# Optimization experiments

Hardware: AMD Instinct MI355X
Metric: run time of the kernel (lower is better)

Reference implementation:

```python
import jax, jax.numpy as jnp
import numpy as np

NG, NC, FG, FC, D = 8192, 4096, 512, 256, 64
ALPHA = 0.2          # leaky_relu negative slope
NEG = -9.0e15        # mask fill value from the torch code


def _leaky(x):
    return jnp.where(x >= 0, x, ALPHA * x)


def _relation(h_src, h_dst, a, adj):
    # additive GAT score: e[i,j] = leaky(h_src[i]@a[:D] + h_dst[j]@a[D:])
    s1 = h_src @ a[:D]            # [Ns]
    s2 = h_dst @ a[D:]            # [Nd]
    e = _leaky(s1[:, None] + s2[None, :])          # [Ns, Nd]
    att = jax.nn.softmax(jnp.where(adj > 0, e, NEG), axis=1)
    return att @ h_dst            # [Ns, D]


def setup_inputs() -> dict:
    key = jax.random.key(0)
    ks = jax.random.split(key, 14)
    sc = 0.05
    return {
        "gene_x": jax.random.normal(ks[0], (NG, FG), jnp.float32),
        "cell_x": jax.random.normal(ks[1], (NC, FC), jnp.float32),
        "W_g": jax.random.normal(ks[2], (FG, D), jnp.float32) * sc,
        "W_c": jax.random.normal(ks[3], (FC, D), jnp.float32) * sc,
        "a_gg": jax.random.normal(ks[4], (2 * D,), jnp.float32) * sc,
        "a_gc": jax.random.normal(ks[5], (2 * D,), jnp.float32) * sc,
        "a_cc": jax.random.normal(ks[6], (2 * D,), jnp.float32) * sc,
        "a_cg": jax.random.normal(ks[7], (2 * D,), jnp.float32) * sc,
        "Wgate_g": jax.random.normal(ks[8], (D, 1), jnp.float32) * sc,
        "bgate_g": jnp.full((1,), -2.0, jnp.float32),
        "Wgate_c": jax.random.normal(ks[9], (D, 1), jnp.float32) * sc,
        "bgate_c": jnp.full((1,), -2.0, jnp.float32),
        "gene_adj": jax.random.randint(ks[10], (NG, NG), 0, 2, jnp.int32),
        "cell_adj": jax.random.randint(ks[11], (NC, NC), 0, 2, jnp.int32),
        "gene_cell_adj": jax.random.randint(ks[12], (NG, NC), 0, 2, jnp.int32),
    }


def reference(gene_x, cell_x, W_g, W_c, a_gg, a_gc, a_cc, a_cg,
              Wgate_g, bgate_g, Wgate_c, bgate_c,
              gene_adj, cell_adj, gene_cell_adj):
    gene_h = gene_x @ W_g                              # [NG, D]
    cell_h = cell_x @ W_c                              # [NC, D]

    gene_from_gene = _relation(gene_h, gene_h, a_gg, gene_adj)
    gene_from_cell = _relation(gene_h, cell_h, a_gc, gene_cell_adj)
    cell_from_cell = _relation(cell_h, cell_h, a_cc, cell_adj)
    cell_from_gene = _relation(cell_h, gene_h, a_cg, gene_cell_adj.T)

    gamma_g = jax.nn.sigmoid(gene_h @ Wgate_g + bgate_g)   # [NG, 1]
    gamma_c = jax.nn.sigmoid(cell_h @ Wgate_c + bgate_c)   # [NC, 1]

    gene_out = _leaky(gene_h + gene_from_gene + gamma_g * gene_from_cell)
    cell_out = _leaky(cell_h + cell_from_cell + gamma_c * cell_from_gene)
    return gene_out, cell_out
```

## Files before the change

kernel.cpp:

```cpp
#include <hip/hip_runtime.h>

#define NG 8192
#define NC 4096
#define FG 512
#define FC 256
#define ALPHA 0.2f

typedef float f32x4 __attribute__((ext_vector_type(4)));
typedef short bf16x8 __attribute__((ext_vector_type(8)));

static __device__ __forceinline__ float leakyf(float x) { return fmaxf(x, ALPHA * x); }

static __device__ __forceinline__ unsigned short f2bf(float f) {
    unsigned u = __builtin_bit_cast(unsigned, f);
    u += 0x7fffu + ((u >> 16) & 1u);
    return (unsigned short)(u >> 16);
}

static __device__ __forceinline__ float wred(float v) {
#pragma unroll
    for (int m = 1; m < 64; m <<= 1) v += __shfl_xor(v, m, 64);
    return v;
}

__global__ __launch_bounds__(256) void proj_kernel(
    const float* __restrict__ x, const float* __restrict__ W, int K, int N,
    float* __restrict__ h, unsigned short* __restrict__ hT,
    const float* __restrict__ aA, const float* __restrict__ aB,
    const float* __restrict__ aC, const float* __restrict__ aD,
    const float* __restrict__ aG, const float* __restrict__ bG,
    float* __restrict__ sA, float* __restrict__ sB, float* __restrict__ sC,
    float* __restrict__ sD, float* __restrict__ gam)
{
    const int wave = threadIdx.x >> 6, lane = threadIdx.x & 63;
    const int r0 = blockIdx.x * 16 + wave * 4;
    const float* xr = x + (size_t)r0 * K;
    float acc0 = 0.f, acc1 = 0.f, acc2 = 0.f, acc3 = 0.f;
    for (int k = 0; k < K; k += 4) {
        float4 x0 = *(const float4*)(xr + k);
        float4 x1 = *(const float4*)(xr + K + k);
        float4 x2 = *(const float4*)(xr + 2 * (size_t)K + k);
        float4 x3 = *(const float4*)(xr + 3 * (size_t)K + k);
        float w0 = W[(k + 0) * 64 + lane];
        float w1 = W[(k + 1) * 64 + lane];
        float w2 = W[(k + 2) * 64 + lane];
        float w3 = W[(k + 3) * 64 + lane];
        acc0 += x0.x * w0 + x0.y * w1 + x0.z * w2 + x0.w * w3;
        acc1 += x1.x * w0 + x1.y * w1 + x1.z * w2 + x1.w * w3;
        acc2 += x2.x * w0 + x2.y * w1 + x2.z * w2 + x2.w * w3;
        acc3 += x3.x * w0 + x3.y * w1 + x3.z * w2 + x3.w * w3;
    }
    float accs[4] = {acc0, acc1, acc2, acc3};
    unsigned short hb[4];
#pragma unroll
    for (int t = 0; t < 4; t++) {
        h[(size_t)(r0 + t) * 64 + lane] = accs[t];
        hb[t] = f2bf(accs[t]);
    }
    *(ushort4*)&hT[(size_t)lane * N + r0] = make_ushort4(hb[0], hb[1], hb[2], hb[3]);

    const float cA = aA[lane], cB = aB[lane], cC = aC[lane], cD = aD[lane], cG = aG[lane];
    const float bias = bG[0];
#pragma unroll
    for (int t = 0; t < 4; t++) {
        float vA = wred(accs[t] * cA);
        float vB = wred(accs[t] * cB);
        float vC = wred(accs[t] * cC);
        float vD = wred(accs[t] * cD);
        float vG = wred(accs[t] * cG);
        if (lane == 0) {
            sA[r0 + t] = vA; sB[r0 + t] = vB; sC[r0 + t] = vC; sD[r0 + t] = vD;
            gam[r0 + t] = 1.f / (1.f + __expf(-(vG + bias)));
        }
    }
}

__global__ __launch_bounds__(256) void rel_kernel(
    const int* __restrict__ adj, int adj_ld, int transposed,
    const float* __restrict__ s1, const float* __restrict__ s2,
    const unsigned short* __restrict__ hT, int Nd,
    float* __restrict__ num, float* __restrict__ lsum, int Ns, int JS)
{
    __shared__ unsigned short lds[64 * 264];
    const int wave = threadIdx.x >> 6, lane = threadIdx.x & 63;
    const int m = lane & 15, kp = lane >> 4;
    const int strip = blockIdx.x, p = blockIdx.y;
    const int jlen = Nd / JS;
    const int jbase = p * jlen;
    const int i_row = strip * 64 + wave * 16 + m;
    const float s1v = s1[i_row];
    f32x4 acc0 = {0.f, 0.f, 0.f, 0.f}, acc1 = acc0, acc2 = acc0, acc3 = acc0;
    float lacc = 0.f;

    for (int j0 = jbase; j0 < jbase + jlen; j0 += 256) {
        for (int idx = threadIdx.x; idx < 2048; idx += 256) {
            int c = idx >> 5, off = (idx & 31) * 8;
            *(int4*)&lds[c * 264 + off] = *(const int4*)&hT[(size_t)c * Nd + j0 + off];
        }
        __syncthreads();
#pragma unroll
        for (int kk = 0; kk < 8; kk++) {
            const int jg = j0 + kk * 32 + kp * 8;
            float s2v[8];
            {
                float4 sa = *(const float4*)&s2[jg];
                float4 sb = *(const float4*)&s2[jg + 4];
                s2v[0] = sa.x; s2v[1] = sa.y; s2v[2] = sa.z; s2v[3] = sa.w;
                s2v[4] = sb.x; s2v[5] = sb.y; s2v[6] = sb.z; s2v[7] = sb.w;
            }
            int am[8];
            if (!transposed) {
                const int* ar = adj + (size_t)i_row * adj_ld + jg;
                int4 a0 = *(const int4*)ar;
                int4 a1 = *(const int4*)(ar + 4);
                am[0] = a0.x; am[1] = a0.y; am[2] = a0.z; am[3] = a0.w;
                am[4] = a1.x; am[5] = a1.y; am[6] = a1.z; am[7] = a1.w;
            } else {
                const int* ac = adj + (size_t)jg * adj_ld + i_row;
#pragma unroll
                for (int t = 0; t < 8; t++) am[t] = ac[(size_t)t * adj_ld];
            }
            bf16x8 af;
#pragma unroll
            for (int t = 0; t < 8; t++) {
                float e = s1v + s2v[t];
                float w = (am[t] > 0) ? __expf(leakyf(e)) : 0.f;
                lacc += w;
                af[t] = (short)f2bf(w);
            }
            const int lb = kk * 32 + kp * 8;
            bf16x8 b0 = *(const bf16x8*)&lds[(0 * 16 + m) * 264 + lb];
            bf16x8 b1 = *(const bf16x8*)&lds[(1 * 16 + m) * 264 + lb];
            bf16x8 b2 = *(const bf16x8*)&lds[(2 * 16 + m) * 264 + lb];
            bf16x8 b3 = *(const bf16x8*)&lds[(3 * 16 + m) * 264 + lb];
            acc0 = __builtin_amdgcn_mfma_f32_16x16x32_bf16(af, b0, acc0, 0, 0, 0);
            acc1 = __builtin_amdgcn_mfma_f32_16x16x32_bf16(af, b1, acc1, 0, 0, 0);
            acc2 = __builtin_amdgcn_mfma_f32_16x16x32_bf16(af, b2, acc2, 0, 0, 0);
            acc3 = __builtin_amdgcn_mfma_f32_16x16x32_bf16(af, b3, acc3, 0, 0, 0);
        }
        __syncthreads();
    }
    const int orow0 = strip * 64 + wave * 16 + kp * 4;
#pragma unroll
    for (int r = 0; r < 4; r++) {
        size_t base = ((size_t)p * Ns + orow0 + r) * 64;
        num[base + m]      = acc0[r];
        num[base + 16 + m] = acc1[r];
        num[base + 32 + m] = acc2[r];
        num[base + 48 + m] = acc3[r];
    }
    lacc += __shfl_xor(lacc, 16, 64);
    lacc += __shfl_xor(lacc, 32, 64);
    if (kp == 0) lsum[(size_t)p * Ns + strip * 64 + wave * 16 + m] = lacc;
}

__global__ __launch_bounds__(256) void combine_store(
    const float* __restrict__ num, const float* __restrict__ l,
    int Ns, int JS, float* __restrict__ R)
{
    int idx = blockIdx.x * 256 + threadIdx.x;
    int i = idx >> 6, c = idx & 63;
    float n = 0.f, d = 0.f;
    for (int p = 0; p < JS; p++) {
        n += num[((size_t)p * Ns + i) * 64 + c];
        d += l[(size_t)p * Ns + i];
    }
    R[idx] = n / d;
}

__global__ __launch_bounds__(256) void combine_final(
    const float* __restrict__ num, const float* __restrict__ l,
    int Ns, int JS, const float* __restrict__ h, const float* __restrict__ Rself,
    const float* __restrict__ gam, float* __restrict__ out)
{
    int idx = blockIdx.x * 256 + threadIdx.x;
    int i = idx >> 6, c = idx & 63;
    float n = 0.f, d = 0.f;
    for (int p = 0; p < JS; p++) {
        n += num[((size_t)p * Ns + i) * 64 + c];
        d += l[(size_t)p * Ns + i];
    }
    float v = h[idx] + Rself[idx] + gam[i] * (n / d);
    out[idx] = leakyf(v);
}

extern "C" void kernel_launch(void* const* d_in, const int* in_sizes, int n_in,
                              void* d_out, int out_size, void* d_ws, size_t ws_size,
                              hipStream_t stream)
{
    const float* gene_x = (const float*)d_in[0];
    const float* cell_x = (const float*)d_in[1];
    const float* W_g    = (const float*)d_in[2];
    const float* W_c    = (const float*)d_in[3];
    const float* a_gg   = (const float*)d_in[4];
    const float* a_gc   = (const float*)d_in[5];
    const float* a_cc   = (const float*)d_in[6];
    const float* a_cg   = (const float*)d_in[7];
    const float* Wgg    = (const float*)d_in[8];
    const float* bgg    = (const float*)d_in[9];
    const float* Wgc    = (const float*)d_in[10];
    const float* bgc    = (const float*)d_in[11];
    const int* gene_adj = (const int*)d_in[12];
    const int* cell_adj = (const int*)d_in[13];
    const int* gc_adj   = (const int*)d_in[14];

    size_t off = 0;
    char* wsb = (char*)d_ws;
    auto alloc = [&](size_t bytes) -> void* {
        void* p = wsb + off;
        off += (bytes + 255) & ~(size_t)255;
        return p;
    };
    float* gene_h = (float*)alloc((size_t)NG * 64 * 4);
    float* cell_h = (float*)alloc((size_t)NC * 64 * 4);
    unsigned short* gene_hT = (unsigned short*)alloc((size_t)NG * 64 * 2);
    unsigned short* cell_hT = (unsigned short*)alloc((size_t)NC * 64 * 2);
    float* s1gg = (float*)alloc(NG * 4);
    float* s2gg = (float*)alloc(NG * 4);
    float* s1gc = (float*)alloc(NG * 4);
    float* s2cg = (float*)alloc(NG * 4);
    float* gamg = (float*)alloc(NG * 4);
    float* s1cc = (float*)alloc(NC * 4);
    float* s2cc = (float*)alloc(NC * 4);
    float* s2gc = (float*)alloc(NC * 4);
    float* s1cg = (float*)alloc(NC * 4);
    float* gamc = (float*)alloc(NC * 4);
    float* Rgg  = (float*)alloc((size_t)NG * 64 * 4);
    float* Rcc  = (float*)alloc((size_t)NC * 64 * 4);
    float* numA = (float*)alloc((size_t)NG * 64 * 4 * 4);
    float* lA   = (float*)alloc((size_t)NG * 4 * 4);
    float* numB = (float*)alloc((size_t)NC * 64 * 8 * 4);
    float* lB   = (float*)alloc((size_t)NC * 8 * 4);

    float* out_gene = (float*)d_out;
    float* out_cell = (float*)d_out + (size_t)NG * 64;

    proj_kernel<<<NG / 16, 256, 0, stream>>>(gene_x, W_g, FG, NG, gene_h, gene_hT,
        a_gg, a_gg + 64, a_gc, a_cg + 64, Wgg, bgg, s1gg, s2gg, s1gc, s2cg, gamg);
    proj_kernel<<<NC / 16, 256, 0, stream>>>(cell_x, W_c, FC, NC, cell_h, cell_hT,
        a_cc, a_cc + 64, a_gc + 64, a_cg, Wgc, bgc, s1cc, s2cc, s2gc, s1cg, gamc);

    rel_kernel<<<dim3(NG / 64, 4), 256, 0, stream>>>(gene_adj, NG, 0, s1gg, s2gg,
        gene_hT, NG, numA, lA, NG, 4);
    combine_store<<<NG * 64 / 256, 256, 0, stream>>>(numA, lA, NG, 4, Rgg);

    rel_kernel<<<dim3(NC / 64, 8), 256, 0, stream>>>(cell_adj, NC, 0, s1cc, s2cc,
        cell_hT, NC, numB, lB, NC, 8);
    combine_store<<<NC * 64 / 256, 256, 0, stream>>>(numB, lB, NC, 8, Rcc);

    rel_kernel<<<dim3(NG / 64, 4), 256, 0, stream>>>(gc_adj, NC, 0, s1gc, s2gc,
        cell_hT, NC, numA, lA, NG, 4);
    rel_kernel<<<dim3(NC / 64, 8), 256, 0, stream>>>(gc_adj, NC, 1, s1cg, s2cg,
        gene_hT, NG, numB, lB, NC, 8);

    combine_final<<<NG * 64 / 256, 256, 0, stream>>>(numA, lA, NG, 4, gene_h, Rgg, gamg, out_gene);
    combine_final<<<NC * 64 / 256, 256, 0, stream>>>(numB, lB, NC, 8, cell_h, Rcc, gamc, out_cell);
}
```

Measured before the change: 741.3 us.

## Raise j-split to 16 for all relations and fold self-term combine into final

Every relation kernel now splits the destination dimension into 16 partitions, with a separate partial buffer per relation. This gives the attention kernels many more blocks to spread across CUs and better hide latency. The separate combine_store pass and the Rgg/Rcc intermediates are removed; combine_final now reduces the self and cross partials in one pass. rel_kernel also gets a min-blocks-per-CU launch bound. The cost is larger partial buffers, more partial traffic in the combine step, and possible register pressure from the occupancy hint.

Result: no change. 729.4 us (-1.6%).

```diff
diff --git a/kernel.cpp b/kernel.cpp
--- a/kernel.cpp
+++ b/kernel.cpp
@@ -75,7 +75,7 @@
     }
 }
 
-__global__ __launch_bounds__(256) void rel_kernel(
+__global__ __launch_bounds__(256, 4) void rel_kernel(
     const int* __restrict__ adj, int adj_ld, int transposed,
     const float* __restrict__ s1, const float* __restrict__ s2,
     const unsigned short* __restrict__ hT, int Nd,
@@ -154,33 +154,24 @@
     if (kp == 0) lsum[(size_t)p * Ns + strip * 64 + wave * 16 + m] = lacc;
 }
 
-__global__ __launch_bounds__(256) void combine_store(
-    const float* __restrict__ num, const float* __restrict__ l,
-    int Ns, int JS, float* __restrict__ R)
+__global__ __launch_bounds__(256) void combine_final(
+    const float* __restrict__ numS, const float* __restrict__ lS, int JSS,
+    const float* __restrict__ numX, const float* __restrict__ lX, int JSX,
+    int Ns, const float* __restrict__ h, const float* __restrict__ gam,
+    float* __restrict__ out)
 {
     int idx = blockIdx.x * 256 + threadIdx.x;
     int i = idx >> 6, c = idx & 63;
-    float n = 0.f, d = 0.f;
-    for (int p = 0; p < JS; p++) {
-        n += num[((size_t)p * Ns + i) * 64 + c];
-        d += l[(size_t)p * Ns + i];
-    }
-    R[idx] = n / d;
-}
-
-__global__ __launch_bounds__(256) void combine_final(
-    const float* __restrict__ num, const float* __restrict__ l,
-    int Ns, int JS, const float* __restrict__ h, const float* __restrict__ Rself,
-    const float* __restrict__ gam, float* __restrict__ out)
-{
-    int idx = blockIdx.x * 256 + threadIdx.x;
-    int i = idx >> 6, c = idx & 63;
-    float n = 0.f, d = 0.f;
-    for (int p = 0; p < JS; p++) {
-        n += num[((size_t)p * Ns + i) * 64 + c];
-        d += l[(size_t)p * Ns + i];
-    }
-    float v = h[idx] + Rself[idx] + gam[i] * (n / d);
+    float nS = 0.f, dS = 0.f, nX = 0.f, dX = 0.f;
+    for (int p = 0; p < JSS; p++) {
+        nS += numS[((size_t)p * Ns + i) * 64 + c];
+        dS += lS[(size_t)p * Ns + i];
+    }
+    for (int p = 0; p < JSX; p++) {
+        nX += numX[((size_t)p * Ns + i) * 64 + c];
+        dX += lX[(size_t)p * Ns + i];
+    }
+    float v = h[idx] + nS / dS + gam[i] * (nX / dX);
     out[idx] = leakyf(v);
 }
 
@@ -211,6 +202,7 @@
         off += (bytes + 255) & ~(size_t)255;
         return p;
     };
+    const int JS = 16;
     float* gene_h = (float*)alloc((size_t)NG * 64 * 4);
     float* cell_h = (float*)alloc((size_t)NC * 64 * 4);
     unsigned short* gene_hT = (unsigned short*)alloc((size_t)NG * 64 * 2);
@@ -225,12 +217,14 @@
     float* s2gc = (float*)alloc(NC * 4);
     float* s1cg = (float*)alloc(NC * 4);
     float* gamc = (float*)alloc(NC * 4);
-    float* Rgg  = (float*)alloc((size_t)NG * 64 * 4);
-    float* Rcc  = (float*)alloc((size_t)NC * 64 * 4);
-    float* numA = (float*)alloc((size_t)NG * 64 * 4 * 4);
-    float* lA   = (float*)alloc((size_t)NG * 4 * 4);
-    float* numB = (float*)alloc((size_t)NC * 64 * 8 * 4);
-    float* lB   = (float*)alloc((size_t)NC * 8 * 4);
+    float* numGG = (float*)alloc((size_t)NG * 64 * JS * 4);
+    float* lGG   = (float*)alloc((size_t)NG * JS * 4);
+    float* numGC = (float*)alloc((size_t)NG * 64 * JS * 4);
+    float* lGC   = (float*)alloc((size_t)NG * JS * 4);
+    float* numCC = (float*)alloc((size_t)NC * 64 * JS * 4);
+    float* lCC   = (float*)alloc((size_t)NC * JS * 4);
+    float* numCG = (float*)alloc((size_t)NC * 64 * JS * 4);
+    float* lCG   = (float*)alloc((size_t)NC * JS * 4);
 
     float* out_gene = (float*)d_out;
     float* out_cell = (float*)d_out + (size_t)NG * 64;
@@ -240,19 +234,17 @@
     proj_kernel<<<NC / 16, 256, 0, stream>>>(cell_x, W_c, FC, NC, cell_h, cell_hT,
         a_cc, a_cc + 64, a_gc + 64, a_cg, Wgc, bgc, s1cc, s2cc, s2gc, s1cg, gamc);
 
-    rel_kernel<<<dim3(NG / 64, 4), 256, 0, stream>>>(gene_adj, NG, 0, s1gg, s2gg,
-        gene_hT, NG, numA, lA, NG, 4);
-    combine_store<<<NG * 64 / 256, 256, 0, stream>>>(numA, lA, NG, 4, Rgg);
-
-    rel_kernel<<<dim3(NC / 64, 8), 256, 0, stream>>>(cell_adj, NC, 0, s1cc, s2cc,
-        cell_hT, NC, numB, lB, NC, 8);
-    combine_store<<<NC * 64 / 256, 256, 0, stream>>>(numB, lB, NC, 8, Rcc);
-
-    rel_kernel<<<dim3(NG / 64, 4), 256, 0, stream>>>(gc_adj, NC, 0, s1gc, s2gc,
-        cell_hT, NC, numA, lA, NG, 4);
-    rel_kernel<<<dim3(NC / 64, 8), 256, 0, stream>>>(gc_adj, NC, 1, s1cg, s2cg,
-        gene_hT, NG, numB, lB, NC, 8);
-
-    combine_final<<<NG * 64 / 256, 256, 0, stream>>>(numA, lA, NG, 4, gene_h, Rgg, gamg, out_gene);
-    combine_final<<<NC * 64 / 256, 256, 0, stream>>>(numB, lB, NC, 8, cell_h, Rcc, gamc, out_cell);
-}
+    rel_kernel<<<dim3(NG / 64, JS), 256, 0, stream>>>(gene_adj, NG, 0, s1gg, s2gg,
+        gene_hT, NG, numGG, lGG, NG, JS);
+    rel_kernel<<<dim3(NC / 64, JS), 256, 0, stream>>>(cell_adj, NC, 0, s1cc, s2cc,
+        cell_hT, NC, numCC, lCC, NC, JS);
+    rel_kernel<<<dim3(NG / 64, JS), 256, 0, stream>>>(gc_adj, NC, 0, s1gc, s2gc,
+        cell_hT, NC, numGC, lGC, NG, JS);
+    rel_kernel<<<dim3(NC / 64, JS), 256, 0, stream>>>(gc_adj, NC, 1, s1cg, s2cg,
+        gene_hT, NG, numCG, lCG, NC, JS);
+
+    combine_final<<<NG * 64 / 256, 256, 0, stream>>>(numGG, lGG, JS, numGC, lGC, JS,
+        NG, gene_h, gamg, out_gene);
+    combine_final<<<NC * 64 / 256, 256, 0, stream>>>(numCC, lCC, JS, numCG, lCG, JS,
+        NC, cell_h, gamc, out_cell);
+}
```
